# Performance work log

Measured on AMD Instinct MI355X. Metric: run time of the kernel, lower is better.

Reference implementation:

```python
import jax, jax.numpy as jnp
import numpy as np

B, D = 8192, 512
NB_CLASSES = 11318
N_EXP = 16
POS_THRESH = 0.25
TOP_K = int(round(B * POS_THRESH))  # plan==1: k = round(B * pos_thresh)


def make_bweights(n):
    # Deterministic init_bweights() from the torch module (17x17 for n=16).
    bw = np.zeros((n + 1, n + 1), dtype=np.float32)
    bw[:, 0] = -1.0 / n
    bw[0, 0] = 1.0
    for i in range(1, n + 1):
        for j in range(1, i):
            bw[i, j] = (-1.0 / n - bw[i] @ bw[j]) / bw[j, j]
        bw[i, i] = np.sqrt(1.0 - np.sum(bw[i, : i + 1] ** 2))
    bw[-1, -1] = 0.0
    return bw


def setup_inputs() -> dict:
    key = jax.random.key(0)
    k1, k2, k3, k4 = jax.random.split(key, 4)
    x_batch = jax.random.normal(k1, (B, D), jnp.float32)
    y_batch = jax.random.randint(k2, (B,), 0, NB_CLASSES)
    # kaiming_normal_ mode='fan_out' on a [nb_classes, sz_embed] tensor: std=sqrt(2/nb_classes)
    proxies = jax.random.normal(k3, (NB_CLASSES, D), jnp.float32) * np.float32(np.sqrt(2.0 / NB_CLASSES))
    rand_units = jax.random.normal(k4, (TOP_K, N_EXP, D), jnp.float32)
    rand_units = rand_units / jnp.linalg.norm(rand_units, axis=-1, keepdims=True)  # gen_unit()
    bweights = jnp.asarray(make_bweights(N_EXP))
    return {"x_batch": x_batch, "y_batch": y_batch, "proxies": proxies,
            "bweights": bweights, "rand_units": rand_units}


def _l2norm(x):
    # torch l2_norm: x / sqrt(sum(x^2, dim=1) + 1e-12)
    return x / jnp.sqrt(jnp.sum(x * x, axis=1, keepdims=True) + 1e-12)


def _expand_one(z, w_c, rands, bweights):
    # one2many_expansion for a single sample. z, w_c: [D]; rands: [N_EXP, D]
    M = jnp.dot(z, w_c) * w_c                 # projection onto class proxy
    r1 = z - M
    r1n = jnp.linalg.norm(r1)
    u1 = r1 / r1n
    # Build orthonormal basis v: [D, N_EXP+2]; columns 0,1 are w_c, u1,
    # columns 2.. via Gram-Schmidt on pre-drawn random unit vectors.
    v = jnp.zeros((D, N_EXP + 2), z.dtype).at[:, 0].set(w_c).at[:, 1].set(u1)
    for i in range(2, N_EXP + 2):  # fixed, small unrolled loop (16 steps)
        r = rands[i - 2]
        nb = r - v[:, :i] @ (v[:, :i].T @ r)  # == sum_j (r.b_j) b_j projection removal
        v = v.at[:, i].set(nb / jnp.linalg.norm(nb))
    # torch: v = v.clone().detach(); v[:,1] = u_1  (only u1 carries gradient)
    v = jax.lax.stop_gradient(v).at[:, 1].set(u1)
    u_rows = bweights @ v[:, 1:].T            # [N_EXP+1, D]
    z_exp = M[None, :] + u_rows * r1n         # [N_EXP+1, D]
    return z_exp[1:]                          # last N_EXP rows


def reference(x_batch, y_batch, proxies, bweights, rand_units):
    X = _l2norm(x_batch)                                  # keep_grad=True
    P = jax.lax.stop_gradient(_l2norm(proxies))           # .clone().detach()
    w = P[y_batch]                                        # [B, D] class proxies
    scores = jnp.sum(X * w, axis=1)                       # z @ P[lb]
    _, top_idx = jax.lax.top_k(scores, TOP_K)
    sel = jnp.sort(top_idx)  # torch loop appends expansions in ascending sample index order
    z_exp = jax.vmap(_expand_one, in_axes=(0, 0, 0, None))(X[sel], w[sel], rand_units, bweights)  # [TOP_K, N_EXP, D]
    lb_exp = jnp.repeat(y_batch[sel], N_EXP)
    aug_x = jnp.concatenate([x_batch, z_exp.reshape(-1, D)], axis=0)
    aug_t = jnp.concatenate([y_batch, lb_exp], axis=0)
    is_expan = jnp.zeros((B,), bool).at[sel].set(True)
    return aug_x, aug_t, is_expan
```

## Files before the change

### kernel.cpp

```cpp
#include <hip/hip_runtime.h>
#include <math.h>

#define BB     8192
#define DD     512
#define NEXP   16
#define TOPK   2048
#define AUGX_ROWS (BB + TOPK * NEXP)
#define AUGT_OFF  ((size_t)AUGX_ROWS * DD)
#define ISEXP_OFF (AUGT_OFF + AUGX_ROWS)

#define JCHUNK 256
#define COPY_BLOCKS 1024
#define BMP 520

typedef __attribute__((ext_vector_type(8)))  short bf16x8;
typedef __attribute__((ext_vector_type(16))) float f32x16;

__device__ inline ushort f2bf(float f) {
    uint u = __builtin_bit_cast(uint, f);
    return (ushort)((u + 0x7FFFu + ((u >> 16) & 1u)) >> 16);
}
__device__ inline float bf2f(ushort b) {
    uint u = ((uint)b) << 16;
    return __builtin_bit_cast(float, u);
}

__global__ __launch_bounds__(256) void score_kernel(
    const float* __restrict__ x, const int* __restrict__ y,
    const float* __restrict__ prox, double* __restrict__ scores,
    float4* __restrict__ hdr, int* __restrict__ ranks)
{
    int wave = threadIdx.x >> 6, lane = threadIdx.x & 63;
    int i = blockIdx.x * 4 + wave;
    const float* xr = x + (size_t)i * DD;
    const float* pr = prox + (size_t)y[i] * DD;
    double sx = 0.0, sp = 0.0, dp = 0.0;
    #pragma unroll
    for (int e = 0; e < DD; e += 64) {
        float xv = xr[e + lane];
        float pv = pr[e + lane];
        sx += (double)xv * (double)xv;
        sp += (double)pv * (double)pv;
        dp += (double)xv * (double)pv;
    }
    #pragma unroll
    for (int off = 32; off > 0; off >>= 1) {
        sx += __shfl_down(sx, off);
        sp += __shfl_down(sp, off);
        dp += __shfl_down(dp, off);
    }
    if (lane == 0) {
        double xn = sqrt(sx + 1e-12), pn = sqrt(sp + 1e-12);
        double zw = dp / (xn * pn);
        scores[i] = zw;
        double r1sq = 1.0 - zw * zw;
        if (r1sq < 1e-12) r1sq = 1e-12;
        float4 h = { (float)xn, (float)pn, (float)zw, (float)sqrt(r1sq) };
        hdr[i] = h;
        ranks[i] = 0;
    }
}

__global__ __launch_bounds__(256) void rank_kernel(
    const double* __restrict__ scores, int* __restrict__ ranks)
{
    __shared__ double ch[JCHUNK];
    int i = blockIdx.x * 256 + threadIdx.x;
    int jbase = blockIdx.y * JCHUNK;
    double si = scores[i];
    if (threadIdx.x < JCHUNK) ch[threadIdx.x] = scores[jbase + threadIdx.x];
    __syncthreads();
    int rank = 0;
    #pragma unroll 8
    for (int j = 0; j < JCHUNK; ++j) {
        double sj = ch[j];
        int jj = jbase + j;
        rank += (sj > si || (sj == si && jj < i)) ? 1 : 0;
    }
    atomicAdd(&ranks[i], rank);
}

__global__ __launch_bounds__(256) void compact_kernel(
    const int* __restrict__ ranks, int* __restrict__ sel, float* __restrict__ out)
{
    __shared__ int wsum[4];
    int t = threadIdx.x;
    int base = t * 32;
    int fl[32];
    int cnt = 0;
    #pragma unroll
    for (int q = 0; q < 8; ++q) {
        int4 rv = *(const int4*)&ranks[base + q * 4];
        fl[q * 4 + 0] = (rv.x < TOPK) ? 1 : 0;
        fl[q * 4 + 1] = (rv.y < TOPK) ? 1 : 0;
        fl[q * 4 + 2] = (rv.z < TOPK) ? 1 : 0;
        fl[q * 4 + 3] = (rv.w < TOPK) ? 1 : 0;
        cnt += fl[q*4] + fl[q*4+1] + fl[q*4+2] + fl[q*4+3];
    }
    int lane = t & 63, wave = t >> 6;
    int inc = cnt;
    #pragma unroll
    for (int off = 1; off < 64; off <<= 1) {
        int n = __shfl_up(inc, off);
        if (lane >= off) inc += n;
    }
    if (lane == 63) wsum[wave] = inc;
    __syncthreads();
    int wbase = 0;
    for (int w = 0; w < wave; ++w) wbase += wsum[w];
    int pos = wbase + inc - cnt;
    #pragma unroll
    for (int q = 0; q < 8; ++q) {
        float4 ev = { fl[q*4] ? 1.0f : 0.0f, fl[q*4+1] ? 1.0f : 0.0f,
                      fl[q*4+2] ? 1.0f : 0.0f, fl[q*4+3] ? 1.0f : 0.0f };
        *(float4*)&out[ISEXP_OFF + base + q * 4] = ev;
        #pragma unroll
        for (int i = 0; i < 4; ++i)
            if (fl[q * 4 + i]) sel[pos++] = base + q * 4 + i;
    }
}

__global__ __launch_bounds__(256, 7) void expand_kernel(
    const float* __restrict__ x, const int* __restrict__ y,
    const float* __restrict__ prox, const float* __restrict__ bwg,
    const float* __restrict__ rands, const int* __restrict__ sel,
    const float4* __restrict__ hdr, float* __restrict__ out)
{
    const int t = threadIdx.x;

    if (blockIdx.x >= TOPK) {
        int tid = (blockIdx.x - TOPK) * 256 + t;
        const float4* src = (const float4*)x;
        float4* dst = (float4*)out;
        const int nvec = BB * DD / 4;
        for (int idx = tid; idx < nvec; idx += COPY_BLOCKS * 256) dst[idx] = src[idx];
        for (int i = tid; i < BB; i += COPY_BLOCKS * 256) out[AUGT_OFF + i] = (float)y[i];
        return;
    }

    __shared__ ushort Bm[18][BMP];
    union SPool {
        float Gp[2][18][19];
        struct { float Ls[18][19]; float Cs[16][18]; } s;
    };
    __shared__ SPool pool;

    const int j = blockIdx.x;
    const int wave = t >> 6, lane = t & 63;
    const int s = sel[j];
    const int cls = y[s];

    {
        const float* rbase = rands + (size_t)j * NEXP * DD;
        #pragma unroll
        for (int i = 0; i < 8; ++i) {
            int row = 2 * i + (t >> 7);
            int col = (t & 127) * 4;
            float4 vv = *(const float4*)(rbase + (size_t)row * DD + col);
            ushort4 bv = { f2bf(vv.x), f2bf(vv.y), f2bf(vv.z), f2bf(vv.w) };
            *(ushort4*)&Bm[2 + row][col] = bv;
        }
    }

    float4 h = hdr[s];
    const float zw = h.z, r1n = h.w;
    const float ixn = 1.0f / h.x, ipn = 1.0f / h.y, ir1 = 1.0f / r1n;

    float2 xv = ((const float2*)(x + (size_t)s * DD))[t];
    float2 pv = ((const float2*)(prox + (size_t)cls * DD))[t];
    float2 w  = { pv.x * ipn, pv.y * ipn };
    float2 z  = { xv.x * ixn, xv.y * ixn };
    float2 M  = { zw * w.x, zw * w.y };
    float2 u1 = { (z.x - M.x) * ir1, (z.y - M.y) * ir1 };

    { ushort2 wb = { f2bf(w.x),  f2bf(w.y)  }; *(ushort2*)&Bm[0][2 * t] = wb; }
    { ushort2 ub = { f2bf(u1.x), f2bf(u1.y) }; *(ushort2*)&Bm[1][2 * t] = ub; }

    if (t < NEXP) out[AUGT_OFF + BB + (size_t)j * NEXP + t] = (float)cls;
    __syncthreads();

    if (wave < 2) {
        int row = lane & 31; if (row > 17) row = 17;
        int koff = (lane >> 5) * 8;
        const int kw = wave * 256;
        f32x16 acc = {0,0,0,0,0,0,0,0,0,0,0,0,0,0,0,0};
        #pragma unroll
        for (int stp = 0; stp < 16; ++stp) {
            bf16x8 av = *(const bf16x8*)&Bm[row][kw + stp * 16 + koff];
            acc = __builtin_amdgcn_mfma_f32_32x32x16_bf16(av, av, acc, 0, 0, 0);
        }
        int col = lane & 31;
        if (col < 18) {
            #pragma unroll
            for (int rg = 0; rg < 16; ++rg) {
                int rr = (rg & 3) + 8 * (rg >> 2) + 4 * (lane >> 5);
                if (rr < 18) pool.Gp[wave][rr][col] = acc[rg];
            }
        }
    }
    __syncthreads();

    if (wave == 0) {
        const int jl = (lane < 18) ? lane : 17;
        float Greg[18];
        #pragma unroll
        for (int c = 0; c < 18; ++c)
            Greg[c] = pool.Gp[0][jl][c] + pool.Gp[1][jl][c];

        float Lrow[18], idr[18];
        #pragma unroll
        for (int col = 0; col < 18; ++col) {
            float pivot = __shfl(Greg[col], col);
            float rsq = rsqrtf(pivot);
            idr[col] = rsq;
            float lv = (jl >= col) ? Greg[col] * rsq : 0.0f;
            Lrow[col] = lv;
            #pragma unroll
            for (int c = col + 1; c < 18; ++c) {
                float lc = __shfl(lv, c);
                Greg[c] -= lv * lc;
            }
        }
        #pragma unroll
        for (int c = 0; c < 18; ++c) pool.s.Ls[jl][c] = Lrow[c];

        if (lane < 16) {
            float b[18];
            b[0] = 0.0f;
            #pragma unroll
            for (int m = 1; m < 18; ++m) b[m] = bwg[17 + lane * 17 + (m - 1)];
            #pragma unroll
            for (int k = 17; k >= 0; --k) {
                float xk = b[k] * idr[k];
                pool.s.Cs[lane][k] = xk;
                #pragma unroll
                for (int m = 0; m < k; ++m)
                    b[m] -= pool.s.Ls[k][m] * xk;
            }
        }
    }
    __syncthreads();

    float bx[18], by[18];
    #pragma unroll
    for (int jj = 0; jj < 18; ++jj) {
        uint v = *(const uint*)&Bm[jj][2 * t];
        bx[jj] = bf2f((ushort)(v & 0xffffu));
        by[jj] = bf2f((ushort)(v >> 16));
    }

    float* orow = out + ((size_t)BB + (size_t)j * NEXP) * DD;
    #pragma unroll
    for (int half = 0; half < 2; ++half) {
        float acc0[8], acc1[8];
        #pragma unroll
        for (int r = 0; r < 8; ++r) { acc0[r] = 0.0f; acc1[r] = 0.0f; }
        #pragma unroll
        for (int jj = 0; jj < 18; ++jj) {
            #pragma unroll
            for (int r = 0; r < 8; ++r) {
                float cc = pool.s.Cs[half * 8 + r][jj];
                acc0[r] += cc * bx[jj];
                acc1[r] += cc * by[jj];
            }
        }
        #pragma unroll
        for (int r = 0; r < 8; ++r) {
            float2 ov = { M.x + r1n * acc0[r], M.y + r1n * acc1[r] };
            ((float2*)(orow + (size_t)(half * 8 + r) * DD))[t] = ov;
        }
    }
}

extern "C" void kernel_launch(void* const* d_in, const int* in_sizes, int n_in,
                              void* d_out, int out_size, void* d_ws, size_t ws_size,
                              hipStream_t stream)
{
    const float* x     = (const float*)d_in[0];
    const int*   y     = (const int*)d_in[1];
    const float* prox  = (const float*)d_in[2];
    const float* bw    = (const float*)d_in[3];
    const float* rands = (const float*)d_in[4];
    float* out = (float*)d_out;

    char* wsb = (char*)d_ws;
    double* scores = (double*)wsb;
    int* ranks = (int*)(wsb + 65536);
    int* sel   = (int*)(wsb + 65536 + 32768);
    float4* hdr = (float4*)(wsb + 114688);

    score_kernel<<<BB / 4, 256, 0, stream>>>(x, y, prox, scores, hdr, ranks);
    dim3 rgrid(BB / 256, BB / JCHUNK);
    rank_kernel<<<rgrid, 256, 0, stream>>>(scores, ranks);
    compact_kernel<<<1, 256, 0, stream>>>(ranks, sel, out);
    expand_kernel<<<TOPK + COPY_BLOCKS, 256, 0, stream>>>(x, y, prox, bw, rands,
                                                          sel, hdr, out);
}
```

Before: 63.97 us.

## Split x passthrough copy between rank and expand kernels

The copy of x_batch and y_batch into the output is split in half. The first half now runs in extra blocks appended to the rank kernel, which is flattened to a 1D grid. The second half stays in the expand kernel with fewer copy blocks. This overlaps part of the 16 MB copy with the rank stage, which underuses bandwidth, and shortens the tail of the expand kernel. The cost is that the rank kernel gets memory traffic competing with its compute.

Result: no change. 65.04 us (+1.7%).

```diff
diff --git a/kernel.cpp b/kernel.cpp
--- a/kernel.cpp
+++ b/kernel.cpp
@@ -10,7 +10,9 @@
 #define ISEXP_OFF (AUGT_OFF + AUGX_ROWS)
 
 #define JCHUNK 256
-#define COPY_BLOCKS 1024
+#define NRANKB 1024
+#define COPYA_BLOCKS 512
+#define COPYB_BLOCKS 512
 #define BMP 520
 
 typedef __attribute__((ext_vector_type(8)))  short bf16x8;
@@ -62,13 +64,27 @@
 }
 
 __global__ __launch_bounds__(256) void rank_kernel(
-    const double* __restrict__ scores, int* __restrict__ ranks)
-{
+    const double* __restrict__ scores, int* __restrict__ ranks,
+    const float* __restrict__ x, const int* __restrict__ y,
+    float* __restrict__ out)
+{
+    const int t = threadIdx.x;
+    if (blockIdx.x >= NRANKB) {
+        int tid = (blockIdx.x - NRANKB) * 256 + t;
+        const float4* src = (const float4*)x;
+        float4* dst = (float4*)out;
+        const int hv = BB * DD / 8;
+        for (int idx = tid; idx < hv; idx += COPYA_BLOCKS * 256) dst[idx] = src[idx];
+        for (int i = tid; i < BB / 2; i += COPYA_BLOCKS * 256)
+            out[AUGT_OFF + i] = (float)y[i];
+        return;
+    }
+
     __shared__ double ch[JCHUNK];
-    int i = blockIdx.x * 256 + threadIdx.x;
-    int jbase = blockIdx.y * JCHUNK;
+    int i = (blockIdx.x & 31) * 256 + t;
+    int jbase = (blockIdx.x >> 5) * JCHUNK;
     double si = scores[i];
-    if (threadIdx.x < JCHUNK) ch[threadIdx.x] = scores[jbase + threadIdx.x];
+    if (t < JCHUNK) ch[t] = scores[jbase + t];
     __syncthreads();
     int rank = 0;
     #pragma unroll 8
@@ -132,9 +148,11 @@
         int tid = (blockIdx.x - TOPK) * 256 + t;
         const float4* src = (const float4*)x;
         float4* dst = (float4*)out;
-        const int nvec = BB * DD / 4;
-        for (int idx = tid; idx < nvec; idx += COPY_BLOCKS * 256) dst[idx] = src[idx];
-        for (int i = tid; i < BB; i += COPY_BLOCKS * 256) out[AUGT_OFF + i] = (float)y[i];
+        const int hv = BB * DD / 8;
+        for (int idx = tid; idx < hv; idx += COPYB_BLOCKS * 256)
+            dst[hv + idx] = src[hv + idx];
+        for (int i = tid; i < BB / 2; i += COPYB_BLOCKS * 256)
+            out[AUGT_OFF + BB / 2 + i] = (float)y[BB / 2 + i];
         return;
     }
 
@@ -290,9 +308,8 @@
     float4* hdr = (float4*)(wsb + 114688);
 
     score_kernel<<<BB / 4, 256, 0, stream>>>(x, y, prox, scores, hdr, ranks);
-    dim3 rgrid(BB / 256, BB / JCHUNK);
-    rank_kernel<<<rgrid, 256, 0, stream>>>(scores, ranks);
+    rank_kernel<<<NRANKB + COPYA_BLOCKS, 256, 0, stream>>>(scores, ranks, x, y, out);
     compact_kernel<<<1, 256, 0, stream>>>(ranks, sel, out);
-    expand_kernel<<<TOPK + COPY_BLOCKS, 256, 0, stream>>>(x, y, prox, bw, rands,
-                                                          sel, hdr, out);
-}
+    expand_kernel<<<TOPK + COPYB_BLOCKS, 256, 0, stream>>>(x, y, prox, bw, rands,
+                                                           sel, hdr, out);
+}
```

## Stage random basis vectors in fp32 LDS via direct global-to-LDS loads

Applied to the files above, without the earlier changes.

Changes the shared basis matrix from bf16 to fp32 and fills the random-vector rows with global_load_lds, so the data goes straight into LDS without passing through registers or being converted at load time. The bf16 conversion moves to the MFMA Gram stage, and the final output combination now reads full-precision basis values. This doubles the LDS footprint per block, and the occupancy hint drops from 7 to 4 blocks. The exchange also brings extra conversion work inside the MFMA loop.

Measured after the change: 63.73 us. No clear change (-0.4%).

```diff
diff --git a/kernel.cpp b/kernel.cpp
--- a/kernel.cpp
+++ b/kernel.cpp
@@ -11,7 +11,7 @@
 
 #define JCHUNK 256
 #define COPY_BLOCKS 1024
-#define BMP 520
+#define FMP 524
 
 typedef __attribute__((ext_vector_type(8)))  short bf16x8;
 typedef __attribute__((ext_vector_type(16))) float f32x16;
@@ -19,10 +19,6 @@
 __device__ inline ushort f2bf(float f) {
     uint u = __builtin_bit_cast(uint, f);
     return (ushort)((u + 0x7FFFu + ((u >> 16) & 1u)) >> 16);
-}
-__device__ inline float bf2f(ushort b) {
-    uint u = ((uint)b) << 16;
-    return __builtin_bit_cast(float, u);
 }
 
 __global__ __launch_bounds__(256) void score_kernel(
@@ -120,7 +116,7 @@
     }
 }
 
-__global__ __launch_bounds__(256, 7) void expand_kernel(
+__global__ __launch_bounds__(256, 4) void expand_kernel(
     const float* __restrict__ x, const int* __restrict__ y,
     const float* __restrict__ prox, const float* __restrict__ bwg,
     const float* __restrict__ rands, const int* __restrict__ sel,
@@ -138,7 +134,7 @@
         return;
     }
 
-    __shared__ ushort Bm[18][BMP];
+    __shared__ float Bm[18][FMP];
     union SPool {
         float Gp[2][18][19];
         struct { float Ls[18][19]; float Cs[16][18]; } s;
@@ -154,11 +150,13 @@
         const float* rbase = rands + (size_t)j * NEXP * DD;
         #pragma unroll
         for (int i = 0; i < 8; ++i) {
-            int row = 2 * i + (t >> 7);
-            int col = (t & 127) * 4;
-            float4 vv = *(const float4*)(rbase + (size_t)row * DD + col);
-            ushort4 bv = { f2bf(vv.x), f2bf(vv.y), f2bf(vv.z), f2bf(vv.w) };
-            *(ushort4*)&Bm[2 + row][col] = bv;
+            int ld = wave + i * 4;
+            int row = ld >> 1, half = ld & 1;
+            const float* g = rbase + (size_t)row * DD + half * 256 + lane * 4;
+            __builtin_amdgcn_global_load_lds(
+                (const __attribute__((address_space(1))) void*)g,
+                (__attribute__((address_space(3))) void*)&Bm[2 + row][half * 256],
+                16, 0, 0);
         }
     }
 
@@ -173,8 +171,8 @@
     float2 M  = { zw * w.x, zw * w.y };
     float2 u1 = { (z.x - M.x) * ir1, (z.y - M.y) * ir1 };
 
-    { ushort2 wb = { f2bf(w.x),  f2bf(w.y)  }; *(ushort2*)&Bm[0][2 * t] = wb; }
-    { ushort2 ub = { f2bf(u1.x), f2bf(u1.y) }; *(ushort2*)&Bm[1][2 * t] = ub; }
+    *(float2*)&Bm[0][2 * t] = w;
+    *(float2*)&Bm[1][2 * t] = u1;
 
     if (t < NEXP) out[AUGT_OFF + BB + (size_t)j * NEXP + t] = (float)cls;
     __syncthreads();
@@ -186,7 +184,14 @@
         f32x16 acc = {0,0,0,0,0,0,0,0,0,0,0,0,0,0,0,0};
         #pragma unroll
         for (int stp = 0; stp < 16; ++stp) {
-            bf16x8 av = *(const bf16x8*)&Bm[row][kw + stp * 16 + koff];
+            int k = kw + stp * 16 + koff;
+            float4 a = *(const float4*)&Bm[row][k];
+            float4 b = *(const float4*)&Bm[row][k + 4];
+            bf16x8 av;
+            av[0] = (short)f2bf(a.x); av[1] = (short)f2bf(a.y);
+            av[2] = (short)f2bf(a.z); av[3] = (short)f2bf(a.w);
+            av[4] = (short)f2bf(b.x); av[5] = (short)f2bf(b.y);
+            av[6] = (short)f2bf(b.z); av[7] = (short)f2bf(b.w);
             acc = __builtin_amdgcn_mfma_f32_32x32x16_bf16(av, av, acc, 0, 0, 0);
         }
         int col = lane & 31;
@@ -244,9 +249,9 @@
     float bx[18], by[18];
     #pragma unroll
     for (int jj = 0; jj < 18; ++jj) {
-        uint v = *(const uint*)&Bm[jj][2 * t];
-        bx[jj] = bf2f((ushort)(v & 0xffffu));
-        by[jj] = bf2f((ushort)(v >> 16));
+        float2 b = *(const float2*)&Bm[jj][2 * t];
+        bx[jj] = b.x;
+        by[jj] = b.y;
     }
 
     float* orow = out + ((size_t)BB + (size_t)j * NEXP) * DD;
```

## Run expand kernel with one wave per block to drop block barriers

Applied to the files above, without the earlier changes.

Each expansion block now uses a single 64-lane wave instead of four waves. The wave does the whole Gram MFMA (split across two accumulators), the Cholesky solve and the output combine, so every __syncthreads and the cross-wave partial-Gram reduction go away. The copy portion gets twice as many blocks to compensate for the smaller block size. In exchange, each thread does four times more per-block work, parallelism within a block drops, and lots of blocks may be limited by LDS occupancy and the launch bound.

New measurement: 131.1 us. 105% more time.

```diff
diff --git a/kernel.cpp b/kernel.cpp
--- a/kernel.cpp
+++ b/kernel.cpp
@@ -10,7 +10,7 @@
 #define ISEXP_OFF (AUGT_OFF + AUGX_ROWS)
 
 #define JCHUNK 256
-#define COPY_BLOCKS 1024
+#define COPY_BLOCKS 2048
 #define BMP 520
 
 typedef __attribute__((ext_vector_type(8)))  short bf16x8;
@@ -120,154 +120,156 @@
     }
 }
 
-__global__ __launch_bounds__(256, 7) void expand_kernel(
+__global__ __launch_bounds__(64, 2) void expand_kernel(
     const float* __restrict__ x, const int* __restrict__ y,
     const float* __restrict__ prox, const float* __restrict__ bwg,
     const float* __restrict__ rands, const int* __restrict__ sel,
     const float4* __restrict__ hdr, float* __restrict__ out)
 {
-    const int t = threadIdx.x;
+    const int lane = threadIdx.x;
 
     if (blockIdx.x >= TOPK) {
-        int tid = (blockIdx.x - TOPK) * 256 + t;
+        int tid = (blockIdx.x - TOPK) * 64 + lane;
         const float4* src = (const float4*)x;
         float4* dst = (float4*)out;
         const int nvec = BB * DD / 4;
-        for (int idx = tid; idx < nvec; idx += COPY_BLOCKS * 256) dst[idx] = src[idx];
-        for (int i = tid; i < BB; i += COPY_BLOCKS * 256) out[AUGT_OFF + i] = (float)y[i];
+        for (int idx = tid; idx < nvec; idx += COPY_BLOCKS * 64) dst[idx] = src[idx];
+        for (int i = tid; i < BB; i += COPY_BLOCKS * 64) out[AUGT_OFF + i] = (float)y[i];
         return;
     }
 
     __shared__ ushort Bm[18][BMP];
-    union SPool {
-        float Gp[2][18][19];
-        struct { float Ls[18][19]; float Cs[16][18]; } s;
-    };
-    __shared__ SPool pool;
+    __shared__ float LsGs[18][19];
+    __shared__ float CsP[16][20];
 
     const int j = blockIdx.x;
-    const int wave = t >> 6, lane = t & 63;
     const int s = sel[j];
     const int cls = y[s];
 
-    {
-        const float* rbase = rands + (size_t)j * NEXP * DD;
-        #pragma unroll
-        for (int i = 0; i < 8; ++i) {
-            int row = 2 * i + (t >> 7);
-            int col = (t & 127) * 4;
-            float4 vv = *(const float4*)(rbase + (size_t)row * DD + col);
-            ushort4 bv = { f2bf(vv.x), f2bf(vv.y), f2bf(vv.z), f2bf(vv.w) };
-            *(ushort4*)&Bm[2 + row][col] = bv;
-        }
+    const float* rbase = rands + (size_t)j * NEXP * DD;
+    #pragma unroll
+    for (int row = 0; row < 16; ++row) {
+        float4 a = *(const float4*)(rbase + row * DD + lane * 4);
+        float4 b = *(const float4*)(rbase + row * DD + 256 + lane * 4);
+        ushort4 la = { f2bf(a.x), f2bf(a.y), f2bf(a.z), f2bf(a.w) };
+        ushort4 lb = { f2bf(b.x), f2bf(b.y), f2bf(b.z), f2bf(b.w) };
+        *(ushort4*)&Bm[2 + row][lane * 4] = la;
+        *(ushort4*)&Bm[2 + row][256 + lane * 4] = lb;
     }
 
     float4 h = hdr[s];
     const float zw = h.z, r1n = h.w;
     const float ixn = 1.0f / h.x, ipn = 1.0f / h.y, ir1 = 1.0f / r1n;
 
-    float2 xv = ((const float2*)(x + (size_t)s * DD))[t];
-    float2 pv = ((const float2*)(prox + (size_t)cls * DD))[t];
-    float2 w  = { pv.x * ipn, pv.y * ipn };
-    float2 z  = { xv.x * ixn, xv.y * ixn };
-    float2 M  = { zw * w.x, zw * w.y };
-    float2 u1 = { (z.x - M.x) * ir1, (z.y - M.y) * ir1 };
-
-    { ushort2 wb = { f2bf(w.x),  f2bf(w.y)  }; *(ushort2*)&Bm[0][2 * t] = wb; }
-    { ushort2 ub = { f2bf(u1.x), f2bf(u1.y) }; *(ushort2*)&Bm[1][2 * t] = ub; }
-
-    if (t < NEXP) out[AUGT_OFF + BB + (size_t)j * NEXP + t] = (float)cls;
-    __syncthreads();
-
-    if (wave < 2) {
+    float2 wv[4];
+    #pragma unroll
+    for (int cc = 0; cc < 4; ++cc) {
+        int d = cc * 128 + lane * 2;
+        float2 xv = *(const float2*)(x + (size_t)s * DD + d);
+        float2 pv = *(const float2*)(prox + (size_t)cls * DD + d);
+        float2 w = { pv.x * ipn, pv.y * ipn };
+        float2 z = { xv.x * ixn, xv.y * ixn };
+        float2 u = { (z.x - zw * w.x) * ir1, (z.y - zw * w.y) * ir1 };
+        wv[cc] = w;
+        ushort2 wb = { f2bf(w.x), f2bf(w.y) };
+        ushort2 ub = { f2bf(u.x), f2bf(u.y) };
+        *(ushort2*)&Bm[0][d] = wb;
+        *(ushort2*)&Bm[1][d] = ub;
+    }
+
+    if (lane < NEXP) out[AUGT_OFF + BB + (size_t)j * NEXP + lane] = (float)cls;
+
+    {
         int row = lane & 31; if (row > 17) row = 17;
         int koff = (lane >> 5) * 8;
-        const int kw = wave * 256;
-        f32x16 acc = {0,0,0,0,0,0,0,0,0,0,0,0,0,0,0,0};
-        #pragma unroll
-        for (int stp = 0; stp < 16; ++stp) {
-            bf16x8 av = *(const bf16x8*)&Bm[row][kw + stp * 16 + koff];
-            acc = __builtin_amdgcn_mfma_f32_32x32x16_bf16(av, av, acc, 0, 0, 0);
+        f32x16 accA = {0,0,0,0,0,0,0,0,0,0,0,0,0,0,0,0};
+        f32x16 accB = {0,0,0,0,0,0,0,0,0,0,0,0,0,0,0,0};
+        #pragma unroll
+        for (int stp = 0; stp < 32; stp += 2) {
+            bf16x8 a0 = *(const bf16x8*)&Bm[row][stp * 16 + koff];
+            bf16x8 a1 = *(const bf16x8*)&Bm[row][(stp + 1) * 16 + koff];
+            accA = __builtin_amdgcn_mfma_f32_32x32x16_bf16(a0, a0, accA, 0, 0, 0);
+            accB = __builtin_amdgcn_mfma_f32_32x32x16_bf16(a1, a1, accB, 0, 0, 0);
         }
         int col = lane & 31;
         if (col < 18) {
             #pragma unroll
             for (int rg = 0; rg < 16; ++rg) {
                 int rr = (rg & 3) + 8 * (rg >> 2) + 4 * (lane >> 5);
-                if (rr < 18) pool.Gp[wave][rr][col] = acc[rg];
+                if (rr < 18) LsGs[rr][col] = accA[rg] + accB[rg];
             }
         }
     }
-    __syncthreads();
-
-    if (wave == 0) {
-        const int jl = (lane < 18) ? lane : 17;
-        float Greg[18];
-        #pragma unroll
-        for (int c = 0; c < 18; ++c)
-            Greg[c] = pool.Gp[0][jl][c] + pool.Gp[1][jl][c];
-
-        float Lrow[18], idr[18];
-        #pragma unroll
-        for (int col = 0; col < 18; ++col) {
-            float pivot = __shfl(Greg[col], col);
-            float rsq = rsqrtf(pivot);
-            idr[col] = rsq;
-            float lv = (jl >= col) ? Greg[col] * rsq : 0.0f;
-            Lrow[col] = lv;
+
+    const int jl = (lane < 18) ? lane : 17;
+    float Greg[18];
+    #pragma unroll
+    for (int c = 0; c < 18; ++c) Greg[c] = LsGs[jl][c];
+
+    float Lrow[18], idr[18];
+    #pragma unroll
+    for (int col = 0; col < 18; ++col) {
+        float pivot = __shfl(Greg[col], col);
+        float rsq = rsqrtf(pivot);
+        idr[col] = rsq;
+        float lv = (jl >= col) ? Greg[col] * rsq : 0.0f;
+        Lrow[col] = lv;
+        #pragma unroll
+        for (int c = col + 1; c < 18; ++c) {
+            float lc = __shfl(lv, c);
+            Greg[c] -= lv * lc;
+        }
+    }
+    #pragma unroll
+    for (int c = 0; c < 18; ++c) LsGs[jl][c] = Lrow[c];
+
+    if (lane < 16) {
+        float b[18];
+        b[0] = 0.0f;
+        #pragma unroll
+        for (int m = 1; m < 18; ++m) b[m] = bwg[17 + lane * 17 + (m - 1)];
+        #pragma unroll
+        for (int k = 17; k >= 0; --k) {
+            float xk = b[k] * idr[k];
+            CsP[lane][k] = xk;
             #pragma unroll
-            for (int c = col + 1; c < 18; ++c) {
-                float lc = __shfl(lv, c);
-                Greg[c] -= lv * lc;
-            }
-        }
-        #pragma unroll
-        for (int c = 0; c < 18; ++c) pool.s.Ls[jl][c] = Lrow[c];
-
-        if (lane < 16) {
-            float b[18];
-            b[0] = 0.0f;
-            #pragma unroll
-            for (int m = 1; m < 18; ++m) b[m] = bwg[17 + lane * 17 + (m - 1)];
-            #pragma unroll
-            for (int k = 17; k >= 0; --k) {
-                float xk = b[k] * idr[k];
-                pool.s.Cs[lane][k] = xk;
-                #pragma unroll
-                for (int m = 0; m < k; ++m)
-                    b[m] -= pool.s.Ls[k][m] * xk;
-            }
-        }
-    }
-    __syncthreads();
-
-    float bx[18], by[18];
-    #pragma unroll
-    for (int jj = 0; jj < 18; ++jj) {
-        uint v = *(const uint*)&Bm[jj][2 * t];
-        bx[jj] = bf2f((ushort)(v & 0xffffu));
-        by[jj] = bf2f((ushort)(v >> 16));
+            for (int m = 0; m < k; ++m)
+                b[m] -= LsGs[k][m] * xk;
+        }
+        CsP[lane][18] = 0.0f; CsP[lane][19] = 0.0f;
     }
 
     float* orow = out + ((size_t)BB + (size_t)j * NEXP) * DD;
     #pragma unroll
-    for (int half = 0; half < 2; ++half) {
-        float acc0[8], acc1[8];
-        #pragma unroll
-        for (int r = 0; r < 8; ++r) { acc0[r] = 0.0f; acc1[r] = 0.0f; }
+    for (int cc = 0; cc < 4; ++cc) {
+        int d = cc * 128 + lane * 2;
+        float bx[18], by[18];
         #pragma unroll
         for (int jj = 0; jj < 18; ++jj) {
-            #pragma unroll
-            for (int r = 0; r < 8; ++r) {
-                float cc = pool.s.Cs[half * 8 + r][jj];
-                acc0[r] += cc * bx[jj];
-                acc1[r] += cc * by[jj];
-            }
-        }
-        #pragma unroll
-        for (int r = 0; r < 8; ++r) {
-            float2 ov = { M.x + r1n * acc0[r], M.y + r1n * acc1[r] };
-            ((float2*)(orow + (size_t)(half * 8 + r) * DD))[t] = ov;
+            uint v = *(const uint*)&Bm[jj][d];
+            bx[jj] = bf2f((ushort)(v & 0xffffu));
+            by[jj] = bf2f((ushort)(v >> 16));
+        }
+        float Mx = zw * wv[cc].x, My = zw * wv[cc].y;
+        #pragma unroll
+        for (int r = 0; r < 16; ++r) {
+            float4 c0 = *(const float4*)&CsP[r][0];
+            float4 c1 = *(const float4*)&CsP[r][4];
+            float4 c2 = *(const float4*)&CsP[r][8];
+            float4 c3 = *(const float4*)&CsP[r][12];
+            float2 c4 = *(const float2*)&CsP[r][16];
+            float a0 = c0.x*bx[0] + c0.y*bx[1] + c0.z*bx[2] + c0.w*bx[3]
+                     + c1.x*bx[4] + c1.y*bx[5] + c1.z*bx[6] + c1.w*bx[7]
+                     + c2.x*bx[8] + c2.y*bx[9] + c2.z*bx[10] + c2.w*bx[11]
+                     + c3.x*bx[12] + c3.y*bx[13] + c3.z*bx[14] + c3.w*bx[15]
+                     + c4.x*bx[16] + c4.y*bx[17];
+            float a1 = c0.x*by[0] + c0.y*by[1] + c0.z*by[2] + c0.w*by[3]
+                     + c1.x*by[4] + c1.y*by[5] + c1.z*by[6] + c1.w*by[7]
+                     + c2.x*by[8] + c2.y*by[9] + c2.z*by[10] + c2.w*by[11]
+                     + c3.x*by[12] + c3.y*by[13] + c3.z*by[14] + c3.w*by[15]
+                     + c4.x*by[16] + c4.y*by[17];
+            float2 ov = { Mx + r1n * a0, My + r1n * a1 };
+            *(float2*)(orow + (size_t)r * DD + d) = ov;
         }
     }
 }
@@ -293,6 +295,6 @@
     dim3 rgrid(BB / 256, BB / JCHUNK);
     rank_kernel<<<rgrid, 256, 0, stream>>>(scores, ranks);
     compact_kernel<<<1, 256, 0, stream>>>(ranks, sel, out);
-    expand_kernel<<<TOPK + COPY_BLOCKS, 256, 0, stream>>>(x, y, prox, bw, rands,
-                                                          sel, hdr, out);
-}
+    expand_kernel<<<TOPK + COPY_BLOCKS, 64, 0, stream>>>(x, y, prox, bw, rands,
+                                                         sel, hdr, out);
+}
```
